# Performance work log

Measured on AMD Instinct MI355X. Metric: run time of the kernel, lower is better.

## Reference

```python
import jax, jax.numpy as jnp
import numpy as np

B, T = 512, 16385  # batch, num_samples; fitted window M = T - 1


def setup_inputs() -> dict:
    key = jax.random.key(0)
    k1, _ = jax.random.split(key)
    # positive samples so ny + cumsum(x) stays > 0 (needed for u**r and log u)
    x = jax.random.uniform(k1, (B, 1, T), dtype=jnp.float32)
    params = jnp.array([0.5, 1.0], dtype=jnp.float32)  # [r, ny]
    return {"x": x, "params": params}


def _cusum(x, h):
    # trapezoidal cumulative integral: y[0]=0, y[t]=y[t-1]+0.5*h*(x[t-1]+x[t])
    inc = 0.5 * h * (x[..., :-1] + x[..., 1:])
    zero = jnp.zeros(x.shape[:-1] + (1,), x.dtype)
    return jnp.concatenate([zero, jnp.cumsum(inc, axis=-1)], axis=-1)


def reference(x, params):
    r, ny = params[0], params[1]
    y = _cusum(x, 1.0)              # (B, 1, T)
    u = ny + y[:, 0, 1:]            # (B, M) ; M = T-1
    phi = jnp.stack([u, u ** r], axis=1)   # (B, 2, M) basis
    phip = jnp.linalg.pinv(phi)            # (B, M, 2)
    xd = x[:, :, 1:]                        # (B, 1, M)
    coeffs = xd @ phip                      # (B, 1, 2)
    x_hat = coeffs @ phi                    # (B, 1, M)
    res = xd - x_hat                        # (B, 1, M)
    r2 = jnp.sum(res ** 2, axis=-1)         # (B, 1)
    return coeffs, x_hat, res, r2
```

## Files before the change

### kernel.cpp

```cpp
#include <hip/hip_runtime.h>
#include <hip/hip_bf16.h>

#define TPB 1024
#define VPT 8
#define TILE (TPB * VPT)
#define NDAT 16384
#define NTILES (NDAT / TILE)
#define TLEN 16385
#define NWAVES (TPB / 64)

__global__ __launch_bounds__(TPB) void vpl_kernel(
    const float* __restrict__ x, const float* __restrict__ params,
    float* __restrict__ out, int B) {
  const int b = blockIdx.x;
  const int tid = threadIdx.x;
  const int lane = tid & 63;
  const int wid = tid >> 6;

  const float r = params[0];
  const float ny = params[1];
  const bool rhalf = (r == 0.5f);

  const float* __restrict__ xr = x + (size_t)b * TLEN;

  float* out_coeffs = out;
  float* out_xhat = out + (size_t)2 * B + (size_t)b * NDAT;
  float* out_res = out + (size_t)2 * B + (size_t)B * NDAT + (size_t)b * NDAT;
  float* out_r2 = out + (size_t)2 * B + (size_t)2 * B * NDAT;

  __shared__ float wt[NTILES][NWAVES];
  __shared__ double sred[NWAVES][5];
  __shared__ float cbc[2];

  double carry = 0.0;
  float offf[NTILES];
  float s_u = 0.f, s_u2 = 0.f, s_u15 = 0.f, s_xu = 0.f, s_xv = 0.f;

#pragma unroll
  for (int k = 0; k < NTILES; ++k) {
    const int base = k * TILE + tid * VPT;
    float xs[VPT + 1];
#pragma unroll
    for (int j = 0; j <= VPT; ++j) xs[j] = xr[base + j];

    float run[VPT];
    float acc = 0.f;
#pragma unroll
    for (int j = 0; j < VPT; ++j) {
      acc += 0.5f * (xs[j] + xs[j + 1]);
      run[j] = acc;
    }
    const float total = acc;

    float t = total;
#pragma unroll
    for (int d = 1; d < 64; d <<= 1) {
      float o = __shfl_up(t, d, 64);
      if (lane >= d) t += o;
    }
    if (lane == 63) wt[k][wid] = t;
    __syncthreads();

    float woff = 0.f, ttot = 0.f;
#pragma unroll
    for (int w = 0; w < NWAVES; ++w) {
      float v = wt[k][w];
      ttot += v;
      if (w < wid) woff += v;
    }
    const float pre = woff + (t - total);
    offf[k] = (float)(carry + (double)ny + (double)pre);

#pragma unroll
    for (int j = 0; j < VPT; ++j) {
      const float uu = offf[k] + run[j];
      const float vh = rhalf ? sqrtf(uu) : powf(uu, r);
      const float xd = xs[j + 1];
      s_u += uu;
      s_u2 = fmaf(uu, uu, s_u2);
      s_u15 = fmaf(uu, vh, s_u15);
      s_xu = fmaf(xd, uu, s_xu);
      s_xv = fmaf(xd, vh, s_xv);
    }
    carry += (double)ttot;
  }

  {
    double vals[5] = {(double)s_u, (double)s_u2, (double)s_u15, (double)s_xu,
                      (double)s_xv};
#pragma unroll
    for (int i = 0; i < 5; ++i) {
      double v = vals[i];
#pragma unroll
      for (int d = 32; d >= 1; d >>= 1) v += __shfl_down(v, d, 64);
      vals[i] = v;
    }
    if (lane == 0) {
#pragma unroll
      for (int i = 0; i < 5; ++i) sred[wid][i] = vals[i];
    }
  }
  __syncthreads();

  if (tid == 0) {
    double g[5];
#pragma unroll
    for (int i = 0; i < 5; ++i) {
      double s = 0.0;
#pragma unroll
      for (int w = 0; w < NWAVES; ++w) s += sred[w][i];
      g[i] = s;
    }
    const double g11 = g[0];
    const double g00 = g[1];
    const double g01 = g[2];
    const double b0 = g[3];
    const double b1 = g[4];

    const double tr = g00 + g11;
    const double det = g00 * g11 - g01 * g01;
    const double disc = sqrt(fmax(tr * tr - 4.0 * det, 0.0));
    const double l1 = 0.5 * (tr + disc);
    const double l2 = (l1 > 0.0) ? fmax(det / l1, 0.0) : 0.0;
    const double s1 = sqrt(fmax(l1, 0.0));
    const double s2 = sqrt(l2);
    const double rcond = 0.01953125;

    double c0, c1;
    if (s2 > rcond * s1) {
      c0 = (g11 * b0 - g01 * b1) / det;
      c1 = (g00 * b1 - g01 * b0) / det;
    } else if (s1 > 0.0) {
      double w0 = l1 - g11, w1 = g01;
      double nrm = sqrt(w0 * w0 + w1 * w1);
      double e0, e1;
      if (nrm > 0.0) {
        e0 = w0 / nrm;
        e1 = w1 / nrm;
      } else {
        e0 = 1.0;
        e1 = 0.0;
      }
      const double gam = (b0 * e0 + b1 * e1) / l1;
      c0 = gam * e0;
      c1 = gam * e1;
    } else {
      c0 = 0.0;
      c1 = 0.0;
    }
    out_coeffs[2 * b] = (float)c0;
    out_coeffs[2 * b + 1] = (float)c1;
    cbc[0] = (float)c0;
    cbc[1] = (float)c1;
  }
  __syncthreads();
  const float c0 = cbc[0];
  const float c1 = cbc[1];

  float r2f = 0.f;
#pragma unroll
  for (int k = 0; k < NTILES; ++k) {
    const int base = k * TILE + tid * VPT;
    float xs[VPT + 1];
#pragma unroll
    for (int j = 0; j <= VPT; ++j) xs[j] = xr[base + j];

    float acc = 0.f;
    float xh[VPT], rs[VPT];
#pragma unroll
    for (int j = 0; j < VPT; ++j) {
      acc += 0.5f * (xs[j] + xs[j + 1]);
      const float uu = offf[k] + acc;
      const float vh = rhalf ? sqrtf(uu) : powf(uu, r);
      xh[j] = fmaf(c0, uu, c1 * vh);
      rs[j] = xs[j + 1] - xh[j];
      r2f = fmaf(rs[j], rs[j], r2f);
    }
    *reinterpret_cast<float4*>(out_xhat + base) =
        make_float4(xh[0], xh[1], xh[2], xh[3]);
    *reinterpret_cast<float4*>(out_xhat + base + 4) =
        make_float4(xh[4], xh[5], xh[6], xh[7]);
    *reinterpret_cast<float4*>(out_res + base) =
        make_float4(rs[0], rs[1], rs[2], rs[3]);
    *reinterpret_cast<float4*>(out_res + base + 4) =
        make_float4(rs[4], rs[5], rs[6], rs[7]);
  }

  double r2 = (double)r2f;
#pragma unroll
  for (int d = 32; d >= 1; d >>= 1) r2 += __shfl_down(r2, d, 64);
  if (lane == 0) sred[wid][0] = r2;
  __syncthreads();
  if (tid == 0) {
    double s = 0.0;
#pragma unroll
    for (int w = 0; w < NWAVES; ++w) s += sred[w][0];
    out_r2[b] = (float)s;
  }
}

extern "C" void kernel_launch(void* const* d_in, const int* in_sizes, int n_in,
                              void* d_out, int out_size, void* d_ws,
                              size_t ws_size, hipStream_t stream) {
  const float* x = (const float*)d_in[0];
  const float* params = (const float*)d_in[1];
  float* out = (float*)d_out;
  const int B = in_sizes[0] / TLEN;
  vpl_kernel<<<dim3(B), dim3(TPB), 0, stream>>>(x, params, out, B);
}
```

Baseline: 107.9 us.

## Keep whole row in registers with 512 threads, dropping the second global read

Each block now runs 512 threads that each own 32 contiguous samples held in registers for the whole kernel. The row is therefore read from global memory once instead of twice, and the two-tile scan with its carry and per-tile barrier becomes a single block scan. The scan now runs in double precision, and the r==0.5 branch is hoisted out of the inner loops into separate sqrt and pow paths. In exchange, register pressure per thread rises a lot and there are half as many threads per block, which may lower occupancy and the latency hiding available for memory traffic.

```diff
diff --git a/kernel.cpp b/kernel.cpp
--- a/kernel.cpp
+++ b/kernel.cpp
@@ -1,13 +1,11 @@
 #include <hip/hip_runtime.h>
 #include <hip/hip_bf16.h>
 
-#define TPB 1024
-#define VPT 8
-#define TILE (TPB * VPT)
+#define TPB 512
+#define VPT 32
 #define NDAT 16384
-#define NTILES (NDAT / TILE)
 #define TLEN 16385
-#define NWAVES (TPB / 64)
+#define NW (TPB / 64)
 
 __global__ __launch_bounds__(TPB) void vpl_kernel(
     const float* __restrict__ x, const float* __restrict__ params,
@@ -28,61 +26,69 @@
   float* out_res = out + (size_t)2 * B + (size_t)B * NDAT + (size_t)b * NDAT;
   float* out_r2 = out + (size_t)2 * B + (size_t)2 * B * NDAT;
 
-  __shared__ float wt[NTILES][NWAVES];
-  __shared__ double sred[NWAVES][5];
+  __shared__ double wtot[NW];
+  __shared__ double sred[NW][5];
   __shared__ float cbc[2];
 
-  double carry = 0.0;
-  float offf[NTILES];
+  const int base = tid * VPT;
+
+  const float x0 = xr[base];
+  float xv[VPT];
+#pragma unroll
+  for (int j = 0; j < VPT; ++j) xv[j] = xr[base + 1 + j];
+
+  float run[VPT];
+  {
+    float prev = x0, acc = 0.f;
+#pragma unroll
+    for (int j = 0; j < VPT; ++j) {
+      acc += 0.5f * (prev + xv[j]);
+      run[j] = acc;
+      prev = xv[j];
+    }
+  }
+  const float tot = run[VPT - 1];
+
+  double t = (double)tot;
+#pragma unroll
+  for (int d = 1; d < 64; d <<= 1) {
+    double o = __shfl_up(t, d, 64);
+    if (lane >= d) t += o;
+  }
+  if (lane == 63) wtot[wid] = t;
+  __syncthreads();
+
+  double cross = 0.0;
+#pragma unroll
+  for (int w = 0; w < NW; ++w)
+    if (w < wid) cross += wtot[w];
+  const float offf = (float)((double)ny + cross + (t - (double)tot));
+
   float s_u = 0.f, s_u2 = 0.f, s_u15 = 0.f, s_xu = 0.f, s_xv = 0.f;
-
-#pragma unroll
-  for (int k = 0; k < NTILES; ++k) {
-    const int base = k * TILE + tid * VPT;
-    float xs[VPT + 1];
-#pragma unroll
-    for (int j = 0; j <= VPT; ++j) xs[j] = xr[base + j];
-
-    float run[VPT];
-    float acc = 0.f;
+  if (rhalf) {
 #pragma unroll
     for (int j = 0; j < VPT; ++j) {
-      acc += 0.5f * (xs[j] + xs[j + 1]);
-      run[j] = acc;
-    }
-    const float total = acc;
-
-    float t = total;
-#pragma unroll
-    for (int d = 1; d < 64; d <<= 1) {
-      float o = __shfl_up(t, d, 64);
-      if (lane >= d) t += o;
-    }
-    if (lane == 63) wt[k][wid] = t;
-    __syncthreads();
-
-    float woff = 0.f, ttot = 0.f;
-#pragma unroll
-    for (int w = 0; w < NWAVES; ++w) {
-      float v = wt[k][w];
-      ttot += v;
-      if (w < wid) woff += v;
-    }
-    const float pre = woff + (t - total);
-    offf[k] = (float)(carry + (double)ny + (double)pre);
-
-#pragma unroll
-    for (int j = 0; j < VPT; ++j) {
-      const float uu = offf[k] + run[j];
-      const float vh = rhalf ? sqrtf(uu) : powf(uu, r);
-      const float xd = xs[j + 1];
+      const float uu = offf + run[j];
+      const float vh = sqrtf(uu);
+      const float xd = xv[j];
       s_u += uu;
       s_u2 = fmaf(uu, uu, s_u2);
       s_u15 = fmaf(uu, vh, s_u15);
       s_xu = fmaf(xd, uu, s_xu);
       s_xv = fmaf(xd, vh, s_xv);
     }
-    carry += (double)ttot;
+  } else {
+#pragma unroll
+    for (int j = 0; j < VPT; ++j) {
+      const float uu = offf + run[j];
+      const float vh = powf(uu, r);
+      const float xd = xv[j];
+      s_u += uu;
+      s_u2 = fmaf(uu, uu, s_u2);
+      s_u15 = fmaf(uu, vh, s_u15);
+      s_xu = fmaf(xd, uu, s_xu);
+      s_xv = fmaf(xd, vh, s_xv);
+    }
   }
 
   {
@@ -108,7 +114,7 @@
     for (int i = 0; i < 5; ++i) {
       double s = 0.0;
 #pragma unroll
-      for (int w = 0; w < NWAVES; ++w) s += sred[w][i];
+      for (int w = 0; w < NW; ++w) s += sred[w][i];
       g[i] = s;
     }
     const double g11 = g[0];
@@ -158,32 +164,42 @@
   const float c1 = cbc[1];
 
   float r2f = 0.f;
-#pragma unroll
-  for (int k = 0; k < NTILES; ++k) {
-    const int base = k * TILE + tid * VPT;
-    float xs[VPT + 1];
-#pragma unroll
-    for (int j = 0; j <= VPT; ++j) xs[j] = xr[base + j];
-
-    float acc = 0.f;
-    float xh[VPT], rs[VPT];
-#pragma unroll
-    for (int j = 0; j < VPT; ++j) {
-      acc += 0.5f * (xs[j] + xs[j + 1]);
-      const float uu = offf[k] + acc;
-      const float vh = rhalf ? sqrtf(uu) : powf(uu, r);
-      xh[j] = fmaf(c0, uu, c1 * vh);
-      rs[j] = xs[j + 1] - xh[j];
-      r2f = fmaf(rs[j], rs[j], r2f);
-    }
-    *reinterpret_cast<float4*>(out_xhat + base) =
-        make_float4(xh[0], xh[1], xh[2], xh[3]);
-    *reinterpret_cast<float4*>(out_xhat + base + 4) =
-        make_float4(xh[4], xh[5], xh[6], xh[7]);
-    *reinterpret_cast<float4*>(out_res + base) =
-        make_float4(rs[0], rs[1], rs[2], rs[3]);
-    *reinterpret_cast<float4*>(out_res + base + 4) =
-        make_float4(rs[4], rs[5], rs[6], rs[7]);
+  if (rhalf) {
+#pragma unroll
+    for (int q = 0; q < VPT / 4; ++q) {
+      float xh[4], rs[4];
+#pragma unroll
+      for (int i = 0; i < 4; ++i) {
+        const int j = q * 4 + i;
+        const float uu = offf + run[j];
+        const float vh = sqrtf(uu);
+        xh[i] = fmaf(c0, uu, c1 * vh);
+        rs[i] = xv[j] - xh[i];
+        r2f = fmaf(rs[i], rs[i], r2f);
+      }
+      *reinterpret_cast<float4*>(out_xhat + base + 4 * q) =
+          make_float4(xh[0], xh[1], xh[2], xh[3]);
+      *reinterpret_cast<float4*>(out_res + base + 4 * q) =
+          make_float4(rs[0], rs[1], rs[2], rs[3]);
+    }
+  } else {
+#pragma unroll
+    for (int q = 0; q < VPT / 4; ++q) {
+      float xh[4], rs[4];
+#pragma unroll
+      for (int i = 0; i < 4; ++i) {
+        const int j = q * 4 + i;
+        const float uu = offf + run[j];
+        const float vh = powf(uu, r);
+        xh[i] = fmaf(c0, uu, c1 * vh);
+        rs[i] = xv[j] - xh[i];
+        r2f = fmaf(rs[i], rs[i], r2f);
+      }
+      *reinterpret_cast<float4*>(out_xhat + base + 4 * q) =
+          make_float4(xh[0], xh[1], xh[2], xh[3]);
+      *reinterpret_cast<float4*>(out_res + base + 4 * q) =
+          make_float4(rs[0], rs[1], rs[2], rs[3]);
+    }
   }
 
   double r2 = (double)r2f;
@@ -194,7 +210,7 @@
   if (tid == 0) {
     double s = 0.0;
 #pragma unroll
-    for (int w = 0; w < NWAVES; ++w) s += sred[w][0];
+    for (int w = 0; w < NW; ++w) s += sred[w][0];
     out_r2[b] = (float)s;
   }
 }
```

New measurement: 119.8 us. 11.0% more time.
